# Performance work log

Measured on AMD Instinct MI355X. Metric: run time of the kernel, lower is better.

Reference implementation:

```python
import jax, jax.numpy as jnp
import numpy as np

D_MODEL = 1024
N_HEADS = 16
HEAD_DIM = D_MODEL // N_HEADS
SEQ_LEN = 2048
D_FF = 4 * D_MODEL
LCC_SCALE = 0.1
LN_EPS = 1e-5
NORM_EPS = 1e-12  # F.normalize eps


def _layer_norm(x, g, b):
    mu = jnp.mean(x, axis=-1, keepdims=True)
    var = jnp.mean(jnp.square(x - mu), axis=-1, keepdims=True)
    return (x - mu) * jax.lax.rsqrt(var + LN_EPS) * g + b


def setup_inputs() -> dict:
    key = jax.random.key(0)
    ks = jax.random.split(key, 8)
    s = 0.02  # weight init scale
    return {
        "x": jax.random.normal(ks[0], (SEQ_LEN, D_MODEL), jnp.float32),
        "lcc_values": jax.random.uniform(ks[1], (SEQ_LEN,), jnp.float32),
        "w_qkv": jax.random.normal(ks[2], (D_MODEL, 3 * D_MODEL), jnp.float32) * s,
        "b_qkv": jnp.zeros((3 * D_MODEL,), jnp.float32),
        "w_out": jax.random.normal(ks[3], (D_MODEL, D_MODEL), jnp.float32) * s,
        "b_out": jnp.zeros((D_MODEL,), jnp.float32),
        "ln1_g": jnp.ones((D_MODEL,), jnp.float32),
        "ln1_b": jnp.zeros((D_MODEL,), jnp.float32),
        "ln2_g": jnp.ones((D_MODEL,), jnp.float32),
        "ln2_b": jnp.zeros((D_MODEL,), jnp.float32),
        "w_ff1": jax.random.normal(ks[4], (D_MODEL, D_FF), jnp.float32) * s,
        "b_ff1": jnp.zeros((D_FF,), jnp.float32),
        "w_ff2": jax.random.normal(ks[5], (D_FF, D_MODEL), jnp.float32) * s,
        "b_ff2": jnp.zeros((D_MODEL,), jnp.float32),
    }


def reference(x, lcc_values, w_qkv, b_qkv, w_out, b_out, ln1_g, ln1_b,
              ln2_g, ln2_b, w_ff1, b_ff1, w_ff2, b_ff2):
    L = x.shape[0]
    scaling = HEAD_DIM ** -0.5

    normed = _layer_norm(x, ln1_g, ln1_b)
    qkv = normed @ w_qkv + b_qkv                      # [L, 3D]
    qkv = qkv.reshape(L, 3, N_HEADS, HEAD_DIM)
    q = jnp.transpose(qkv[:, 0], (1, 0, 2))           # [H, L, d]
    k = jnp.transpose(qkv[:, 1], (1, 0, 2))
    v = jnp.transpose(qkv[:, 2], (1, 0, 2))

    # cosine attention: L2-normalize q, k
    q = q / jnp.maximum(jnp.linalg.norm(q, axis=-1, keepdims=True), NORM_EPS)
    k = k / jnp.maximum(jnp.linalg.norm(k, axis=-1, keepdims=True), NORM_EPS)
    q = q * scaling

    scores = jnp.einsum('hld,hmd->hlm', q, k)         # [H, L, L]
    bias = (lcc_values[:, None] + lcc_values[None, :]) * 0.5 * LCC_SCALE
    scores = jnp.clip(scores + bias[None], -10.0, 10.0)
    probs = jax.nn.softmax(scores, axis=-1)

    attn = jnp.einsum('hlm,hmd->hld', probs, v)       # [H, L, d]
    attn = jnp.transpose(attn, (1, 0, 2)).reshape(L, D_MODEL)
    x = x + (attn @ w_out + b_out)

    normed2 = _layer_norm(x, ln2_g, ln2_b)
    h = jax.nn.gelu(normed2 @ w_ff1 + b_ff1, approximate=False)
    x = x + (h @ w_ff2 + b_ff2)
    return x
```

## Files before the change

### kernel.cpp

```cpp
#include <hip/hip_runtime.h>
#include <hip/hip_bf16.h>

#define D_MODEL 1024
#define SEQ 2048
#define NH 16
#define HD 64
#define DFF 4096

typedef __attribute__((ext_vector_type(8))) __bf16 bf16x8;
typedef __attribute__((ext_vector_type(4))) float f32x4;

__device__ __forceinline__ unsigned short f2bf(float f) {
    union { float f; unsigned u; } v; v.f = f;
    unsigned r = v.u + 0x7fffu + ((v.u >> 16) & 1u);
    return (unsigned short)(r >> 16);
}
__device__ __forceinline__ unsigned pack2(float a, float b) {
    return (unsigned)f2bf(a) | ((unsigned)f2bf(b) << 16);
}
__device__ __forceinline__ float bf2f(unsigned short u) {
    union { unsigned u; float f; } v; v.u = ((unsigned)u) << 16;
    return v.f;
}
__device__ __forceinline__ bf16x8 ld_frag(const unsigned short* p) {
    union { uint4 u; bf16x8 b; } c;
    c.u = *(const uint4*)p;
    return c.b;
}

typedef __attribute__((address_space(3))) unsigned lds_u32;
typedef const __attribute__((address_space(1))) unsigned glob_u32;
__device__ __forceinline__ void gl_lds16(const unsigned short* g, unsigned short* l) {
    __builtin_amdgcn_global_load_lds((glob_u32*)g, (lds_u32*)l, 16, 0, 0);
}

#define MFMA16(a,b,c) __builtin_amdgcn_mfma_f32_16x16x32_bf16(a,b,c,0,0,0)

__global__ __launch_bounds__(256) void wcast_all(const float* __restrict__ wq, const float* __restrict__ wo,
                                                 const float* __restrict__ wf1, const float* __restrict__ wf2,
                                                 unsigned short* __restrict__ oq, unsigned short* __restrict__ oo,
                                                 unsigned short* __restrict__ of1, unsigned short* __restrict__ of2) {
    __shared__ unsigned short lt[64][72];
    int id = blockIdx.x;
    const float* W; unsigned short* O; int K, N, nb, kb;
    if (id < 768)       { W = wq;  O = oq;  K = 1024; N = 3072; nb = id % 48; kb = id / 48; }
    else if (id < 1024) { id -= 768;  W = wo;  O = oo;  K = 1024; N = 1024; nb = id & 15; kb = id >> 4; }
    else if (id < 2048) { id -= 1024; W = wf1; O = of1; K = 1024; N = 4096; nb = id & 63; kb = id >> 6; }
    else                { id -= 2048; W = wf2; O = of2; K = 4096; N = 1024; nb = id & 15; kb = id >> 4; }
    int t = threadIdx.x;
    int r = t >> 2, c0 = (t & 3) << 4;
    const float* src = W + (size_t)(kb*64 + r) * N + nb*64 + c0;
    float4 f0 = ((const float4*)src)[0];
    float4 f1 = ((const float4*)src)[1];
    float4 f2 = ((const float4*)src)[2];
    float4 f3 = ((const float4*)src)[3];
    unsigned* dst = (unsigned*)&lt[r][c0];
    dst[0]=pack2(f0.x,f0.y); dst[1]=pack2(f0.z,f0.w);
    dst[2]=pack2(f1.x,f1.y); dst[3]=pack2(f1.z,f1.w);
    dst[4]=pack2(f2.x,f2.y); dst[5]=pack2(f2.z,f2.w);
    dst[6]=pack2(f3.x,f3.y); dst[7]=pack2(f3.z,f3.w);
    __syncthreads();
    int n_ = t >> 2, k0 = (t & 3) << 4;
    unsigned obuf[8];
#pragma unroll
    for (int i = 0; i < 8; i++)
        obuf[i] = (unsigned)lt[k0 + 2*i][n_] | ((unsigned)lt[k0 + 2*i + 1][n_] << 16);
    unsigned short* out = O + (size_t)(nb*64 + n_) * K + kb*64 + k0;
    ((uint4*)out)[0] = *(uint4*)&obuf[0];
    ((uint4*)out)[1] = *(uint4*)&obuf[4];
}

__global__ __launch_bounds__(256) void ln_kernel(const float* __restrict__ x,
                                                 const float* __restrict__ g,
                                                 const float* __restrict__ b,
                                                 unsigned short* __restrict__ out) {
    int row = blockIdx.x, t = threadIdx.x;
    float4 v = ((const float4*)(x + (size_t)row * D_MODEL))[t];
    float s  = v.x + v.y + v.z + v.w;
    float sq = v.x*v.x + v.y*v.y + v.z*v.z + v.w*v.w;
#pragma unroll
    for (int m = 1; m < 64; m <<= 1) { s += __shfl_xor(s, m, 64); sq += __shfl_xor(sq, m, 64); }
    __shared__ float ls[4], lq[4];
    int wave = t >> 6, lane = t & 63;
    if (lane == 0) { ls[wave] = s; lq[wave] = sq; }
    __syncthreads();
    s  = ls[0]+ls[1]+ls[2]+ls[3];
    sq = lq[0]+lq[1]+lq[2]+lq[3];
    float mu  = s * (1.0f / D_MODEL);
    float var = sq * (1.0f / D_MODEL) - mu * mu;
    float rs  = rsqrtf(var + 1e-5f);
    int c = t * 4;
    float y0 = (v.x - mu) * rs * g[c+0] + b[c+0];
    float y1 = (v.y - mu) * rs * g[c+1] + b[c+1];
    float y2 = (v.z - mu) * rs * g[c+2] + b[c+2];
    float y3 = (v.w - mu) * rs * g[c+3] + b[c+3];
    unsigned* o = (unsigned*)(out + (size_t)row * D_MODEL + c);
    o[0] = pack2(y0, y1); o[1] = pack2(y2, y3);
}

__global__ __launch_bounds__(256) void reduce_ln(const float* __restrict__ x,
                                                 const float* __restrict__ bout,
                                                 const unsigned short* __restrict__ parts,
                                                 const float* __restrict__ g,
                                                 const float* __restrict__ b,
                                                 float* __restrict__ x1,
                                                 unsigned short* __restrict__ x2n) {
    int row = blockIdx.x, t = threadIdx.x;
    int i = row * 256 + t;
    float4 v = ((const float4*)x)[i];
    float4 bb = ((const float4*)bout)[t];
    v.x += bb.x; v.y += bb.y; v.z += bb.z; v.w += bb.w;
#pragma unroll
    for (int p = 0; p < 4; p++) {
        ushort4 u = ((const ushort4*)(parts + (size_t)p * SEQ * D_MODEL))[i];
        v.x += bf2f(u.x); v.y += bf2f(u.y); v.z += bf2f(u.z); v.w += bf2f(u.w);
    }
    ((float4*)x1)[i] = v;
    float s  = v.x + v.y + v.z + v.w;
    float sq = v.x*v.x + v.y*v.y + v.z*v.z + v.w*v.w;
#pragma unroll
    for (int m = 1; m < 64; m <<= 1) { s += __shfl_xor(s, m, 64); sq += __shfl_xor(sq, m, 64); }
    __shared__ float ls[4], lq[4];
    int wave = t >> 6, lane = t & 63;
    if (lane == 0) { ls[wave] = s; lq[wave] = sq; }
    __syncthreads();
    s  = ls[0]+ls[1]+ls[2]+ls[3];
    sq = lq[0]+lq[1]+lq[2]+lq[3];
    float mu  = s * (1.0f / D_MODEL);
    float var = sq * (1.0f / D_MODEL) - mu * mu;
    float rs  = rsqrtf(var + 1e-5f);
    int c = t * 4;
    float y0 = (v.x - mu) * rs * g[c+0] + b[c+0];
    float y1 = (v.y - mu) * rs * g[c+1] + b[c+1];
    float y2 = (v.z - mu) * rs * g[c+2] + b[c+2];
    float y3 = (v.w - mu) * rs * g[c+3] + b[c+3];
    unsigned* o = (unsigned*)(x2n + (size_t)row * D_MODEL + c);
    o[0] = pack2(y0, y1); o[1] = pack2(y2, y3);
}

__global__ __launch_bounds__(256) void reduce_ff2(const float* __restrict__ res,
                                                  const float* __restrict__ bias,
                                                  const unsigned short* __restrict__ parts,
                                                  float* __restrict__ out) {
    int i = blockIdx.x * 256 + threadIdx.x;
    float4 r = ((const float4*)res)[i];
    float4 b = ((const float4*)bias)[i & (D_MODEL/4 - 1)];
    r.x += b.x; r.y += b.y; r.z += b.z; r.w += b.w;
#pragma unroll
    for (int p = 0; p < 4; p++) {
        ushort4 u = ((const ushort4*)(parts + (size_t)p * SEQ * D_MODEL))[i];
        r.x += bf2f(u.x); r.y += bf2f(u.y); r.z += bf2f(u.z); r.w += bf2f(u.w);
    }
    ((float4*)out)[i] = r;
}

#define TMg 128
#define TNg 128
#define HALFg ((TMg + TNg) * 64)
#define SMEM_U16 (2 * HALFg)
__device__ __forceinline__ void gemm_core512(const unsigned short* __restrict__ A,
                                             const unsigned short* __restrict__ Bt,
                                             int K, int K0, int KS, int bm, int bn,
                                             unsigned short* smem, f32x4 acc[4][4],
                                             int w, int lane) {
    int quad = lane >> 4, lr = lane & 15;
    int kg = w >> 2;
    const unsigned short* pa[2]; const unsigned short* pb[2];
    int aoff[2], boff[2];
#pragma unroll
    for (int i = 0; i < 2; i++) {
        int rl = i*64 + w*8 + (lane >> 3);
        int sc = (lane & 7) ^ (rl & 7);
        pa[i] = A  + (size_t)(bm*TMg + rl) * K + K0 + sc*8;
        pb[i] = Bt + (size_t)(bn*TNg + rl) * K + K0 + sc*8;
        aoff[i] = (i*64 + w*8) * 64;
        boff[i] = TMg*64 + (i*64 + w*8) * 64;
    }
    int wr = ((w >> 1) & 1) * 64, wc = (w & 1) * 64;
    int foA[4], foB[4];
#pragma unroll
    for (int i = 0; i < 4; i++) {
        int ra = wr + i*16 + lr;
        foA[i] = ra*64 + (((quad + 4*kg) ^ (ra & 7)))*8;
        int rb = wc + i*16 + lr;
        foB[i] = TMg*64 + rb*64 + (((quad + 4*kg) ^ (rb & 7)))*8;
    }
#pragma unroll
    for (int i = 0; i < 2; i++) { gl_lds16(pa[i], smem + aoff[i]); gl_lds16(pb[i], smem + boff[i]); }
    int bo = 0;
    int T = KS >> 6;
    for (int t = 0; t < T; t++) {
        __syncthreads();
        if (t + 1 < T) {
            int nb = bo ^ HALFg;
#pragma unroll
            for (int i = 0; i < 2; i++) {
                gl_lds16(pa[i] + (t+1)*64, smem + nb + aoff[i]);
                gl_lds16(pb[i] + (t+1)*64, smem + nb + boff[i]);
            }
        }
        const unsigned short* s = smem + bo;
        bf16x8 af[4], bfr[4];
#pragma unroll
        for (int i = 0; i < 4; i++) af[i] = ld_frag(s + foA[i]);
#pragma unroll
        for (int j = 0; j < 4; j++) bfr[j] = ld_frag(s + foB[j]);
        __builtin_amdgcn_s_setprio(1);
#pragma unroll
        for (int i = 0; i < 4; i++)
#pragma unroll
            for (int j = 0; j < 4; j++)
                acc[i][j] = MFMA16(af[i], bfr[j], acc[i][j]);
        __builtin_amdgcn_s_setprio(0);
        bo ^= HALFg;
    }
}

__device__ __forceinline__ void acc_init(f32x4 acc[4][4]) {
    f32x4 z = {0.f, 0.f, 0.f, 0.f};
#pragma unroll
    for (int i = 0; i < 4; i++)
#pragma unroll
        for (int j = 0; j < 4; j++) acc[i][j] = z;
}

__device__ __forceinline__ void acc_merge_split(unsigned short* smem, f32x4 acc[4][4],
                                                int w, int lane) {
    float* X = (float*)smem;
    int kg = w >> 2, p = w & 3, quad = lane >> 4, lr = lane & 15;
    if (kg) {
#pragma unroll
        for (int i = 0; i < 4; i++) {
            f32x4 t0 = acc[i][0]; acc[i][0] = acc[i][2]; acc[i][2] = t0;
            f32x4 t1 = acc[i][1]; acc[i][1] = acc[i][3]; acc[i][3] = t1;
        }
    }
    __syncthreads();
    int g = (kg ^ 1) * 2;
#pragma unroll
    for (int i = 0; i < 4; i++)
#pragma unroll
        for (int r = 0; r < 4; r++) {
            int ro = (i*16 + r*4 + quad)*16 + lr;
            X[(p*4 + g    )*1024 + ro] = acc[i][2][r];
            X[(p*4 + g + 1)*1024 + ro] = acc[i][3][r];
        }
    __syncthreads();
    int k = kg * 2;
#pragma unroll
    for (int i = 0; i < 4; i++)
#pragma unroll
        for (int r = 0; r < 4; r++) {
            int ro = (i*16 + r*4 + quad)*16 + lr;
            acc[i][0][r] += X[(p*4 + k    )*1024 + ro];
            acc[i][1][r] += X[(p*4 + k + 1)*1024 + ro];
        }
}

__global__ __launch_bounds__(512, 4) void k_gemm_qkv(const unsigned short* __restrict__ A,
                                                     const unsigned short* __restrict__ Bt,
                                                     const float* __restrict__ bias,
                                                     unsigned short* __restrict__ qn,
                                                     unsigned short* __restrict__ kn,
                                                     unsigned short* __restrict__ vt) {
    __shared__ unsigned short smem[SMEM_U16];
    int t = threadIdx.x;
    int bn = blockIdx.x, bm = blockIdx.y;
    int w = t >> 6, lane = t & 63;
    int quad = lane >> 4, lr = lane & 15;
    f32x4 acc[4][4];
    acc_init(acc);
    gemm_core512(A, Bt, 1024, 0, 1024, bm, bn, smem, acc, w, lane);

    float* X = (float*)smem;
    int kg = w >> 2, p = w & 3;
    __syncthreads();
    if (kg == 1) {
#pragma unroll
        for (int j = 0; j < 4; j++) {
            float* slot = X + (p*4 + j)*1024;
#pragma unroll
            for (int i = 0; i < 4; i++)
#pragma unroll
                for (int r = 0; r < 4; r++)
                    slot[(i*16 + r*4 + quad)*16 + lr] = acc[i][j][r];
        }
    }
    __syncthreads();
    int wr = ((w >> 1) & 1) * 64, wc = (w & 1) * 64;
    int sec = bn >> 3, hp = bn & 7;
    if (kg == 0) {
#pragma unroll
        for (int j = 0; j < 4; j++) {
            const float* slot = X + (p*4 + j)*1024;
            float bv = bias[bn*TNg + wc + j*16 + lr];
#pragma unroll
            for (int i = 0; i < 4; i++)
#pragma unroll
                for (int r = 0; r < 4; r++)
                    acc[i][j][r] += slot[(i*16 + r*4 + quad)*16 + lr] + bv;
        }
    }

    if (sec < 2) {
        if (kg == 0) {
            int h = hp*2 + (w & 1);
            unsigned short* dst = (sec == 0) ? qn : kn;
            float mul = (sec == 0) ? 0.125f : 1.0f;
#pragma unroll
            for (int i = 0; i < 4; i++)
#pragma unroll
                for (int r = 0; r < 4; r++) {
                    float ss = 0.f;
#pragma unroll
                    for (int j = 0; j < 4; j++) ss += acc[i][j][r]*acc[i][j][r];
                    ss += __shfl_xor(ss, 1, 64); ss += __shfl_xor(ss, 2, 64);
                    ss += __shfl_xor(ss, 4, 64); ss += __shfl_xor(ss, 8, 64);
                    float scale = mul / fmaxf(sqrtf(ss), 1e-12f);
                    int row = bm*TMg + wr + i*16 + quad*4 + r;
                    size_t base = ((size_t)h*SEQ + row) * HD;
#pragma unroll
                    for (int j = 0; j < 4; j++)
                        dst[base + j*16 + lr] = f2bf(acc[i][j][r] * scale);
                }
        }
    } else {
        __syncthreads();
        unsigned short (*lv)[136] = (unsigned short (*)[136])smem;
        if (kg == 0) {
#pragma unroll
            for (int i = 0; i < 4; i++)
#pragma unroll
                for (int j = 0; j < 4; j++)
#pragma unroll
                    for (int r = 0; r < 4; r++)
                        lv[wc + j*16 + lr][wr + i*16 + quad*4 + r] = f2bf(acc[i][j][r]);
        }
        __syncthreads();
        int d = t >> 2, l0 = (t & 3) * 32;
        unsigned short* ov = vt + ((size_t)(hp*128 + d)) * SEQ + bm*TMg + l0;
#pragma unroll
        for (int c = 0; c < 4; c++)
            ((uint4*)ov)[c] = *(uint4*)&lv[d][l0 + c*8];
    }
}

template<int SPLITK>
__device__ __forceinline__ void gemm_part512(const unsigned short* A, const unsigned short* Bt,
                                             unsigned short* C, int M, int N, int K) {
    __shared__ unsigned short smem[SMEM_U16];
    int t = threadIdx.x;
    int bn = blockIdx.x, bm = blockIdx.y, kz = blockIdx.z;
    int w = t >> 6, lane = t & 63;
    int quad = lane >> 4, lr = lane & 15;
    int KS = K / SPLITK;
    f32x4 acc[4][4];
    acc_init(acc);
    gemm_core512(A, Bt, K, kz*KS, KS, bm, bn, smem, acc, w, lane);
    acc_merge_split(smem, acc, w, lane);
    int kg = w >> 2, wr = ((w >> 1) & 1) * 64, wc = (w & 1) * 64;
    unsigned short* P = C + (size_t)kz * M * N;
    int col0 = bn*TNg + wc + (kg*2)*16 + lr;
    int col1 = col0 + 16;
#pragma unroll
    for (int i = 0; i < 4; i++) {
        int row0 = bm*TMg + wr + i*16 + quad*4;
#pragma unroll
        for (int r = 0; r < 4; r++) {
            P[(size_t)(row0 + r) * N + col0] = f2bf(acc[i][0][r]);
            P[(size_t)(row0 + r) * N + col1] = f2bf(acc[i][1][r]);
        }
    }
}
__global__ __launch_bounds__(512, 4) void k_gemm_op(const unsigned short* A, const unsigned short* Bt,
                                                    unsigned short* C, int M, int N, int K) {
    gemm_part512<4>(A, Bt, C, M, N, K);
}
__global__ __launch_bounds__(512, 4) void k_gemm_ff2(const unsigned short* A, const unsigned short* Bt,
                                                     unsigned short* C, int M, int N, int K) {
    gemm_part512<4>(A, Bt, C, M, N, K);
}

__global__ __launch_bounds__(512, 4) void k_gemm_ff1(const unsigned short* __restrict__ A,
                                                     const unsigned short* __restrict__ Bt,
                                                     const float* __restrict__ bias,
                                                     unsigned short* __restrict__ C,
                                                     int M, int N, int K) {
    __shared__ unsigned short smem[SMEM_U16];
    int t = threadIdx.x;
    int bn = blockIdx.x, bm = blockIdx.y;
    int w = t >> 6, lane = t & 63;
    int quad = lane >> 4, lr = lane & 15;
    f32x4 acc[4][4];
    acc_init(acc);
    gemm_core512(A, Bt, K, 0, K, bm, bn, smem, acc, w, lane);
    acc_merge_split(smem, acc, w, lane);
    int kg = w >> 2, wr = ((w >> 1) & 1) * 64, wc = (w & 1) * 64;
    int col0 = bn*TNg + wc + (kg*2)*16 + lr;
    int col1 = col0 + 16;
    float bv0 = bias[col0], bv1 = bias[col1];
#pragma unroll
    for (int i = 0; i < 4; i++) {
        int row0 = bm*TMg + wr + i*16 + quad*4;
#pragma unroll
        for (int r = 0; r < 4; r++) {
            float v0 = acc[i][0][r] + bv0;
            v0 = 0.5f * v0 * (1.0f + erff(v0 * 0.70710678118654752f));
            C[(size_t)(row0 + r) * N + col0] = f2bf(v0);
            float v1 = acc[i][1][r] + bv1;
            v1 = 0.5f * v1 * (1.0f + erff(v1 * 0.70710678118654752f));
            C[(size_t)(row0 + r) * N + col1] = f2bf(v1);
        }
    }
}

#define KSPLIT 2
#define KTILES (SEQ / 64 / KSPLIT)
__global__ __launch_bounds__(256) void attn_kernel(const unsigned short* __restrict__ qn,
                                                   const unsigned short* __restrict__ kn,
                                                   const unsigned short* __restrict__ vt,
                                                   const float* __restrict__ lcc,
                                                   float* __restrict__ num_ws,
                                                   float* __restrict__ den_ws) {
    __shared__ unsigned short lQP[64*64];
    __shared__ unsigned short lK[2][64*64];
    __shared__ unsigned short lV[2][64*64];
    int h = blockIdx.x, qb = blockIdx.y, kz = blockIdx.z;
    int t = threadIdx.x;
    int wave = t >> 6, lane = t & 63, quad = lane >> 4, lr = lane & 15;
    int r0 = lane >> 3;
    int ch = lane & 7;

    const unsigned short* kn0 = kn + (size_t)h*SEQ*HD + (size_t)kz*(SEQ/KSPLIT)*HD;
    const unsigned short* vt0 = vt + (size_t)h*HD*SEQ + kz*(SEQ/KSPLIT);
    const float* lcc0 = lcc + kz*(SEQ/KSPLIT);

#pragma unroll
    for (int i = 0; i < 2; i++) {
        int rl = wave*16 + i*8 + r0;
        int ss = ch ^ (rl & 7);
        gl_lds16(qn + ((size_t)h*SEQ + qb*64 + rl)*HD + ss*8, lQP + (wave*16 + i*8)*64);
        gl_lds16(kn0 + (size_t)rl*HD + ss*8,                  lK[0] + (wave*16 + i*8)*64);
        gl_lds16(vt0 + (size_t)rl*SEQ + ss*8,                 lV[0] + (wave*16 + i*8)*64);
    }
    __syncthreads();

    bf16x8 aq0 = ld_frag(lQP + (wave*16 + lr)*64 + ((quad     ^ (lr & 7)))*8);
    bf16x8 aq1 = ld_frag(lQP + (wave*16 + lr)*64 + (((quad+4) ^ (lr & 7)))*8);

    f32x4 z = {0.f, 0.f, 0.f, 0.f};
    f32x4 oacc[4]; oacc[0]=z; oacc[1]=z; oacc[2]=z; oacc[3]=z;
    float den[4] = {0.f, 0.f, 0.f, 0.f};

    int cur = 0;
    for (int kb = 0; kb < KTILES; kb++) {
        if (kb + 1 < KTILES) {
            int nxt = cur ^ 1;
#pragma unroll
            for (int i = 0; i < 2; i++) {
                int rl = wave*16 + i*8 + r0;
                int ss = ch ^ (rl & 7);
                gl_lds16(kn0 + (size_t)(kb+1)*64*HD + (size_t)rl*HD + ss*8,
                         lK[nxt] + (wave*16 + i*8)*64);
                gl_lds16(vt0 + (size_t)rl*SEQ + (kb+1)*64 + ss*8,
                         lV[nxt] + (wave*16 + i*8)*64);
            }
        }
        float lmv[4];
#pragma unroll
        for (int j = 0; j < 4; j++) lmv[j] = 0.05f * lcc0[kb*64 + j*16 + lr];

        __builtin_amdgcn_s_setprio(1);
        const unsigned short* Kc = lK[cur];
#pragma unroll
        for (int j = 0; j < 4; j++) {
            bf16x8 b0 = ld_frag(Kc + (j*16 + lr)*64 + ((quad     ^ (lr & 7)))*8);
            bf16x8 b1 = ld_frag(Kc + (j*16 + lr)*64 + (((quad+4) ^ (lr & 7)))*8);
            f32x4 s = z;
            s = MFMA16(aq0, b0, s);
            s = MFMA16(aq1, b1, s);
#pragma unroll
            for (int r = 0; r < 4; r++) {
                float p = __expf(s[r] + lmv[j]);
                den[r] += p;
                int prow = wave*16 + quad*4 + r;
                lQP[prow*64 + (((2*j + (lr >> 3)) ^ (prow & 7)))*8 + (lr & 7)] = f2bf(p);
            }
        }
        bf16x8 ap0 = ld_frag(lQP + (wave*16 + lr)*64 + ((quad     ^ (lr & 7)))*8);
        bf16x8 ap1 = ld_frag(lQP + (wave*16 + lr)*64 + (((quad+4) ^ (lr & 7)))*8);
        const unsigned short* Vc = lV[cur];
#pragma unroll
        for (int j2 = 0; j2 < 4; j2++) {
            bf16x8 b0 = ld_frag(Vc + (j2*16 + lr)*64 + ((quad     ^ (lr & 7)))*8);
            bf16x8 b1 = ld_frag(Vc + (j2*16 + lr)*64 + (((quad+4) ^ (lr & 7)))*8);
            oacc[j2] = MFMA16(ap0, b0, oacc[j2]);
            oacc[j2] = MFMA16(ap1, b1, oacc[j2]);
        }
        __builtin_amdgcn_s_setprio(0);
        __syncthreads();
        cur ^= 1;
    }
#pragma unroll
    for (int r = 0; r < 4; r++)
#pragma unroll
        for (int m = 1; m < 16; m <<= 1) den[r] += __shfl_xor(den[r], m, 64);

    float* nump = num_ws + (((size_t)(h*32 + qb)) * KSPLIT + kz) * 4096;
#pragma unroll
    for (int j2 = 0; j2 < 4; j2++)
#pragma unroll
        for (int r = 0; r < 4; r++)
            nump[(wave*16 + quad*4 + r) * 64 + j2*16 + lr] = oacc[j2][r];
    if (lr == 0) {
        float* denp = den_ws + (((size_t)(h*32 + qb)) * KSPLIT + kz) * 64;
#pragma unroll
        for (int r = 0; r < 4; r++) denp[wave*16 + quad*4 + r] = den[r];
    }
}

__global__ __launch_bounds__(256) void attn_comb(const float* __restrict__ num_ws,
                                                 const float* __restrict__ den_ws,
                                                 unsigned short* __restrict__ attn) {
    int hq = blockIdx.x;
    int h = hq >> 5, qb = hq & 31;
    int t = threadIdx.x;
    int row = t >> 2, col0 = (t & 3) << 4;
    const float* n0 = num_ws + ((size_t)hq * KSPLIT) * 4096 + row*64 + col0;
    const float* n1 = n0 + 4096;
    float d = den_ws[(size_t)hq * KSPLIT * 64 + row] + den_ws[((size_t)hq * KSPLIT + 1) * 64 + row];
    float inv = 1.0f / d;
    unsigned ob[8];
#pragma unroll
    for (int i = 0; i < 4; i++) {
        float4 a = ((const float4*)n0)[i];
        float4 b = ((const float4*)n1)[i];
        ob[2*i]   = pack2((a.x + b.x) * inv, (a.y + b.y) * inv);
        ob[2*i+1] = pack2((a.z + b.z) * inv, (a.w + b.w) * inv);
    }
    unsigned short* op = attn + (size_t)(qb*64 + row) * D_MODEL + h*64 + col0;
    ((uint4*)op)[0] = *(uint4*)&ob[0];
    ((uint4*)op)[1] = *(uint4*)&ob[4];
}

extern "C" void kernel_launch(void* const* d_in, const int* in_sizes, int n_in,
                              void* d_out, int out_size, void* d_ws, size_t ws_size,
                              hipStream_t stream) {
    const float* x      = (const float*)d_in[0];
    const float* lcc    = (const float*)d_in[1];
    const float* w_qkv  = (const float*)d_in[2];
    const float* b_qkv  = (const float*)d_in[3];
    const float* w_out  = (const float*)d_in[4];
    const float* b_out  = (const float*)d_in[5];
    const float* ln1_g  = (const float*)d_in[6];
    const float* ln1_b  = (const float*)d_in[7];
    const float* ln2_g  = (const float*)d_in[8];
    const float* ln2_b  = (const float*)d_in[9];
    const float* w_ff1  = (const float*)d_in[10];
    const float* b_ff1  = (const float*)d_in[11];
    const float* w_ff2  = (const float*)d_in[12];
    const float* b_ff2  = (const float*)d_in[13];

    char* ws = (char*)d_ws;
    unsigned short* wtq  = (unsigned short*)(ws);
    unsigned short* wto  = (unsigned short*)(ws + 6291456);
    unsigned short* wtf1 = (unsigned short*)(ws + 8388608);
    unsigned short* wtf2 = (unsigned short*)(ws + 16777216);
    unsigned short* xn   = (unsigned short*)(ws + 25165824);
    float*          x1   = (float*)(ws + 29360128);
    float*          numw = (float*)(ws + 29360128);
    float*          denw = (float*)(ws + 46137344);
    unsigned short* hbuf = (unsigned short*)(ws + 37748736);
    unsigned short* pOP  = (unsigned short*)(ws + 37748736);
    unsigned short* qnb  = (unsigned short*)(ws + 54525952);
    unsigned short* knb  = (unsigned short*)(ws + 58720256);
    unsigned short* vtb  = (unsigned short*)(ws + 62914560);
    unsigned short* pFF2 = (unsigned short*)(ws);
    unsigned short* attnb = xn;
    unsigned short* x2n  = qnb;
    float* outp = (float*)d_out;


    wcast_all<<<3072, 256, 0, stream>>>(w_qkv, w_out, w_ff1, w_ff2, wtq, wto, wtf1, wtf2);
    ln_kernel<<<SEQ, 256, 0, stream>>>(x, ln1_g, ln1_b, xn);
    k_gemm_qkv<<<dim3(24, 16), 512, 0, stream>>>(xn, wtq, b_qkv, qnb, knb, vtb);
    attn_kernel<<<dim3(16, 32, KSPLIT), 256, 0, stream>>>(qnb, knb, vtb, lcc, numw, denw);
    attn_comb<<<512, 256, 0, stream>>>(numw, denw, attnb);
    k_gemm_op<<<dim3(8, 16, 4), 512, 0, stream>>>(attnb, wto, pOP, SEQ, 1024, 1024);
    reduce_ln<<<SEQ, 256, 0, stream>>>(x, b_out, pOP, ln2_g, ln2_b, x1, x2n);
    k_gemm_ff1<<<dim3(32, 16), 512, 0, stream>>>(x2n, wtf1, b_ff1, hbuf, SEQ, 4096, 1024);
    k_gemm_ff2<<<dim3(8, 16, 4), 512, 0, stream>>>(hbuf, wtf2, pFF2, SEQ, 1024, 4096);
    reduce_ff2<<<SEQ*D_MODEL/1024, 256, 0, stream>>>(x1, b_ff2, pFF2, outp);
}
```

Measured before the change: 261.8 us.

## Use 256x256 tiles with 4-stage half-K pipeline for FF1 and FF2 GEMMs

Replaces the 128x128 intra-block split-K GEMM core for the two FFN GEMMs with a 256x256 block tile. Each wave holds a 128x64 accumulator, and the K dimension is staged in 32-wide chunks through four LDS buffers with direct global-to-LDS loads and priority hints around the MFMA bursts. The aim is more data reuse per LDS byte and the removal of the cross-wave accumulator merge. In exchange, per-wave register pressure is much higher and the grids are smaller (128 blocks for FF1, 128 for FF2), which may leave CUs underused on a 256-CU device.

```diff
diff --git a/kernel.cpp b/kernel.cpp
--- a/kernel.cpp
+++ b/kernel.cpp
@@ -154,6 +154,142 @@
     ((float4*)out)[i] = r;
 }
 
+#define BMh 256
+#define BNh 256
+#define SMEM8_U16 65536
+
+__device__ __forceinline__ void acc_init8(f32x4 acc[8][4]) {
+    f32x4 z = {0.f, 0.f, 0.f, 0.f};
+#pragma unroll
+    for (int i = 0; i < 8; i++)
+#pragma unroll
+        for (int j = 0; j < 4; j++) acc[i][j] = z;
+}
+
+__device__ __forceinline__ void issue_half(const unsigned short* gA0, const unsigned short* gA1,
+                                           const unsigned short* gB0, const unsigned short* gB1,
+                                           unsigned short* smem, int s,
+                                           int dA0, int dA1, int dB0, int dB1) {
+    unsigned short* db = smem + ((s >> 1) & 1) * 32768 + (s & 1) * 8192;
+    gl_lds16(gA0 + s*32, db + dA0);
+    gl_lds16(gA1 + s*32, db + dA1);
+    gl_lds16(gB0 + s*32, db + 16384 + dB0);
+    gl_lds16(gB1 + s*32, db + 16384 + dB1);
+}
+
+__device__ __forceinline__ void gemm_core8ph(const unsigned short* __restrict__ A,
+                                             const unsigned short* __restrict__ Bt,
+                                             int K, int K0, int KS, int bm, int bn,
+                                             unsigned short* smem, f32x4 acc[8][4],
+                                             int w, int lane) {
+    int quad = lane >> 4, lr = lane & 15;
+    int wm = w >> 2, wn = w & 3;
+    int t = w*64 + lane;
+    int srow = t >> 2, sch = t & 3;
+    int r0 = srow, r1 = 128 + srow;
+    int sc = sch ^ (r0 & 3);
+    const unsigned short* gA0 = A  + (size_t)(bm*BMh + r0) * K + K0 + sc*8;
+    const unsigned short* gA1 = A  + (size_t)(bm*BMh + r1) * K + K0 + sc*8;
+    const unsigned short* gB0 = Bt + (size_t)(bn*BNh + r0) * K + K0 + sc*8;
+    const unsigned short* gB1 = Bt + (size_t)(bn*BNh + r1) * K + K0 + sc*8;
+    int dA0 = r0*32 + sch*8, dA1 = r1*32 + sch*8;
+    int foA[8], foB[4];
+#pragma unroll
+    for (int i = 0; i < 8; i++) { int ra = wm*128 + i*16 + lr; foA[i] = ra*32 + ((quad ^ (ra & 3)))*8; }
+#pragma unroll
+    for (int j = 0; j < 4; j++) { int rb = wn*64 + j*16 + lr; foB[j] = rb*32 + ((quad ^ (rb & 3)))*8; }
+
+    int T2 = KS >> 5;
+    issue_half(gA0, gA1, gB0, gB1, smem, 0, dA0, dA1, dA0, dA1);
+    issue_half(gA0, gA1, gB0, gB1, smem, 1, dA0, dA1, dA0, dA1);
+    for (int s = 0; s < T2; s++) {
+        if (s + 1 < T2) asm volatile("s_waitcnt vmcnt(4)" ::: "memory");
+        else            asm volatile("s_waitcnt vmcnt(0)" ::: "memory");
+        __builtin_amdgcn_s_barrier();
+        if (s + 2 < T2) issue_half(gA0, gA1, gB0, gB1, smem, s + 2, dA0, dA1, dA0, dA1);
+        const unsigned short* sa = smem + ((s >> 1) & 1) * 32768 + (s & 1) * 8192;
+        const unsigned short* sb = sa + 16384;
+        bf16x8 bfr[4], af0[4], af1[4];
+#pragma unroll
+        for (int j = 0; j < 4; j++) bfr[j] = ld_frag(sb + foB[j]);
+#pragma unroll
+        for (int i = 0; i < 4; i++) af0[i] = ld_frag(sa + foA[i]);
+        __builtin_amdgcn_s_setprio(1);
+#pragma unroll
+        for (int i = 0; i < 4; i++)
+#pragma unroll
+            for (int j = 0; j < 4; j++)
+                acc[i][j] = MFMA16(af0[i], bfr[j], acc[i][j]);
+        __builtin_amdgcn_s_setprio(0);
+#pragma unroll
+        for (int i = 0; i < 4; i++) af1[i] = ld_frag(sa + foA[4 + i]);
+        __builtin_amdgcn_s_setprio(1);
+#pragma unroll
+        for (int i = 0; i < 4; i++)
+#pragma unroll
+            for (int j = 0; j < 4; j++)
+                acc[4 + i][j] = MFMA16(af1[i], bfr[j], acc[4 + i][j]);
+        __builtin_amdgcn_s_setprio(0);
+    }
+}
+
+__global__ __launch_bounds__(512, 2) void k_gemm_ff1(const unsigned short* __restrict__ A,
+                                                     const unsigned short* __restrict__ Bt,
+                                                     const float* __restrict__ bias,
+                                                     unsigned short* __restrict__ C,
+                                                     int M, int N, int K) {
+    __shared__ unsigned short smem[SMEM8_U16];
+    int t = threadIdx.x, w = t >> 6, lane = t & 63;
+    int bn = blockIdx.x, bm = blockIdx.y;
+    int quad = lane >> 4, lr = lane & 15;
+    f32x4 acc[8][4];
+    acc_init8(acc);
+    gemm_core8ph(A, Bt, K, 0, K, bm, bn, smem, acc, w, lane);
+    int wm = w >> 2, wn = w & 3;
+#pragma unroll
+    for (int j = 0; j < 4; j++) {
+        int col = bn*BNh + wn*64 + j*16 + lr;
+        float bvv = bias[col];
+#pragma unroll
+        for (int i = 0; i < 8; i++) {
+            int row0 = bm*BMh + wm*128 + i*16 + quad*4;
+#pragma unroll
+            for (int r = 0; r < 4; r++) {
+                float v = acc[i][j][r] + bvv;
+                v = 0.5f * v * (1.0f + erff(v * 0.70710678118654752f));
+                C[(size_t)(row0 + r) * N + col] = f2bf(v);
+            }
+        }
+    }
+}
+
+__global__ __launch_bounds__(512, 2) void k_gemm_ff2(const unsigned short* __restrict__ A,
+                                                     const unsigned short* __restrict__ Bt,
+                                                     unsigned short* __restrict__ C,
+                                                     int M, int N, int K) {
+    __shared__ unsigned short smem[SMEM8_U16];
+    int t = threadIdx.x, w = t >> 6, lane = t & 63;
+    int bn = blockIdx.x, bm = blockIdx.y, kz = blockIdx.z;
+    int quad = lane >> 4, lr = lane & 15;
+    int KS = K >> 2;
+    f32x4 acc[8][4];
+    acc_init8(acc);
+    gemm_core8ph(A, Bt, K, kz*KS, KS, bm, bn, smem, acc, w, lane);
+    int wm = w >> 2, wn = w & 3;
+    unsigned short* P = C + (size_t)kz * M * N;
+#pragma unroll
+    for (int j = 0; j < 4; j++) {
+        int col = bn*BNh + wn*64 + j*16 + lr;
+#pragma unroll
+        for (int i = 0; i < 8; i++) {
+            int row0 = bm*BMh + wm*128 + i*16 + quad*4;
+#pragma unroll
+            for (int r = 0; r < 4; r++)
+                P[(size_t)(row0 + r) * N + col] = f2bf(acc[i][j][r]);
+        }
+    }
+}
+
 #define TMg 128
 #define TNg 128
 #define HALFg ((TMg + TNg) * 64)
@@ -375,43 +511,6 @@
 __global__ __launch_bounds__(512, 4) void k_gemm_op(const unsigned short* A, const unsigned short* Bt,
                                                     unsigned short* C, int M, int N, int K) {
     gemm_part512<4>(A, Bt, C, M, N, K);
-}
-__global__ __launch_bounds__(512, 4) void k_gemm_ff2(const unsigned short* A, const unsigned short* Bt,
-                                                     unsigned short* C, int M, int N, int K) {
-    gemm_part512<4>(A, Bt, C, M, N, K);
-}
-
-__global__ __launch_bounds__(512, 4) void k_gemm_ff1(const unsigned short* __restrict__ A,
-                                                     const unsigned short* __restrict__ Bt,
-                                                     const float* __restrict__ bias,
-                                                     unsigned short* __restrict__ C,
-                                                     int M, int N, int K) {
-    __shared__ unsigned short smem[SMEM_U16];
-    int t = threadIdx.x;
-    int bn = blockIdx.x, bm = blockIdx.y;
-    int w = t >> 6, lane = t & 63;
-    int quad = lane >> 4, lr = lane & 15;
-    f32x4 acc[4][4];
-    acc_init(acc);
-    gemm_core512(A, Bt, K, 0, K, bm, bn, smem, acc, w, lane);
-    acc_merge_split(smem, acc, w, lane);
-    int kg = w >> 2, wr = ((w >> 1) & 1) * 64, wc = (w & 1) * 64;
-    int col0 = bn*TNg + wc + (kg*2)*16 + lr;
-    int col1 = col0 + 16;
-    float bv0 = bias[col0], bv1 = bias[col1];
-#pragma unroll
-    for (int i = 0; i < 4; i++) {
-        int row0 = bm*TMg + wr + i*16 + quad*4;
-#pragma unroll
-        for (int r = 0; r < 4; r++) {
-            float v0 = acc[i][0][r] + bv0;
-            v0 = 0.5f * v0 * (1.0f + erff(v0 * 0.70710678118654752f));
-            C[(size_t)(row0 + r) * N + col0] = f2bf(v0);
-            float v1 = acc[i][1][r] + bv1;
-            v1 = 0.5f * v1 * (1.0f + erff(v1 * 0.70710678118654752f));
-            C[(size_t)(row0 + r) * N + col1] = f2bf(v1);
-        }
-    }
 }
 
 #define KSPLIT 2
@@ -588,7 +687,7 @@
     attn_comb<<<512, 256, 0, stream>>>(numw, denw, attnb);
     k_gemm_op<<<dim3(8, 16, 4), 512, 0, stream>>>(attnb, wto, pOP, SEQ, 1024, 1024);
     reduce_ln<<<SEQ, 256, 0, stream>>>(x, b_out, pOP, ln2_g, ln2_b, x1, x2n);
-    k_gemm_ff1<<<dim3(32, 16), 512, 0, stream>>>(x2n, wtf1, b_ff1, hbuf, SEQ, 4096, 1024);
-    k_gemm_ff2<<<dim3(8, 16, 4), 512, 0, stream>>>(hbuf, wtf2, pFF2, SEQ, 1024, 4096);
+    k_gemm_ff1<<<dim3(16, 8), 512, 0, stream>>>(x2n, wtf1, b_ff1, hbuf, SEQ, 4096, 1024);
+    k_gemm_ff2<<<dim3(4, 8, 4), 512, 0, stream>>>(hbuf, wtf2, pFF2, SEQ, 1024, 4096);
     reduce_ff2<<<SEQ*D_MODEL/1024, 256, 0, stream>>>(x1, b_ff2, pFF2, outp);
 }
```

After: 286.3 us. 1.09x slower.
